# Optimization experiments

Hardware: AMD Instinct MI355X
Metric: run time of the kernel (lower is better)

## Reference

```python
import jax, jax.numpy as jnp
import numpy as np

DIM = 128
HEADS = 4
GN_GROUPS = 4
EPS = 1e-5


def setup_inputs() -> dict:
    key = jax.random.key(0)
    ks = jax.random.split(key, 6)
    B, C, H, W = 4, DIM, 64, 64
    x = jax.random.normal(ks[0], (B, C, H, W), dtype=jnp.float32)
    # 1x1 convs are channel matmuls: store as [out_ch, in_ch]
    w_qkv = jax.random.normal(ks[1], (3 * C, C), dtype=jnp.float32) * (C ** -0.5)
    w_out = jax.random.normal(ks[2], (C, C), dtype=jnp.float32) * (C ** -0.5)
    b_out = jax.random.normal(ks[3], (C,), dtype=jnp.float32) * 0.01
    gn_gamma = jnp.ones((C,), dtype=jnp.float32)
    gn_beta = jnp.zeros((C,), dtype=jnp.float32)
    return {"x": x, "w_qkv": w_qkv, "w_out": w_out, "b_out": b_out,
            "gn_gamma": gn_gamma, "gn_beta": gn_beta}


def _attention_block(x, w_qkv, w_out, b_out, gn_gamma, gn_beta):
    b, c, h, w = x.shape
    d = c // HEADS
    scale = d ** -0.5
    # 1x1 conv == per-pixel matmul over channels
    qkv = jnp.einsum('bchw,oc->bohw', x, w_qkv)  # [b, 3c, h, w]
    q, k, v = jnp.split(qkv, 3, axis=1)
    # 'b (h d) x y -> b h (x y) d'
    def to_heads(t):
        return t.reshape(b, HEADS, d, h * w).transpose(0, 1, 3, 2)  # [b, H, N, d]
    q, k, v = to_heads(q), to_heads(k), to_heads(v)
    dots = jnp.einsum('bhnd,bhmd->bhnm', q, k) * scale  # [b, H, N, N]
    attn = jax.nn.softmax(dots, axis=-1)
    out = jnp.einsum('bhnm,bhmd->bhnd', attn, v)  # [b, H, N, d]
    # 'b h (x y) d -> b (h d) x y'
    out = out.transpose(0, 1, 3, 2).reshape(b, c, h, w)
    # output 1x1 conv + bias
    out = jnp.einsum('bchw,oc->bohw', out, w_out) + b_out[None, :, None, None]
    # GroupNorm(4, c)
    g = out.reshape(b, GN_GROUPS, c // GN_GROUPS, h, w)
    mean = g.mean(axis=(2, 3, 4), keepdims=True)
    var = g.var(axis=(2, 3, 4), keepdims=True)
    g = (g - mean) * jax.lax.rsqrt(var + EPS)
    out = g.reshape(b, c, h, w) * gn_gamma[None, :, None, None] + gn_beta[None, :, None, None]
    return out + x


def reference(x, w_qkv, w_out, b_out, gn_gamma, gn_beta):
    return _attention_block(x, w_qkv, w_out, b_out, gn_gamma, gn_beta)
```

## Files before the change

### kernel.cpp

```cpp
#include <hip/hip_runtime.h>

#define DIM   128
#define NPIX  4096
#define DHEAD 32

using u16 = unsigned short;
typedef __attribute__((ext_vector_type(8))) short   short8;
typedef __attribute__((ext_vector_type(8))) u16     ushort8;
typedef __attribute__((ext_vector_type(4))) float   floatx4;
typedef __attribute__((ext_vector_type(2))) unsigned int uint2v;

#define SCL 0.25513899f

__device__ __forceinline__ float bf2f(u16 u) {
  union { unsigned int i; float f; } v; v.i = ((unsigned int)u) << 16; return v.f;
}
__device__ __forceinline__ u16 f2bf(float f) {
  union { unsigned int i; float f; } v; v.f = f;
  unsigned int i = v.i;
  return (u16)((i + 0x7FFFu + ((i >> 16) & 1u)) >> 16);
}
__device__ __forceinline__ unsigned int pk2bf(float a, float b) {
  union { float f; unsigned int u; } ua, ub; ua.f = a; ub.f = b;
  return __builtin_amdgcn_perm(ub.u, ua.u, 0x07060302u);
}

template<bool F32> __device__ __forceinline__ float ld1(const void* p, size_t i) {
  if constexpr (F32) return ((const float*)p)[i];
  else               return bf2f(((const u16*)p)[i]);
}
template<bool F32> __device__ __forceinline__ float4 ld4(const void* p, size_t i) {
  if constexpr (F32) {
    return *(const float4*)((const float*)p + i);
  } else {
    const ushort4 u = *(const ushort4*)((const u16*)p + i);
    return make_float4(bf2f(u.x), bf2f(u.y), bf2f(u.z), bf2f(u.w));
  }
}
template<bool F32> __device__ __forceinline__ void st4(void* p, size_t i, float4 v) {
  if constexpr (F32) {
    *(float4*)((float*)p + i) = v;
  } else {
    ushort4 u; u.x = f2bf(v.x); u.y = f2bf(v.y); u.z = f2bf(v.z); u.w = f2bf(v.w);
    *(ushort4*)((u16*)p + i) = u;
  }
}

__global__ void k_detect(const u16* __restrict__ x, int* __restrict__ flag,
                         float* __restrict__ S) {
  if (threadIdx.x < 40) S[threadIdx.x] = 0.f;
  if (threadIdx.x == 0 && blockIdx.x == 0) {
    int big = 0;
    for (int i = 0; i < 128; ++i) {
      const float v = bf2f(x[i]);
      if (!(fabsf(v) < 1e4f)) big = 1;
    }
    *flag = big;
  }
}

template<bool F32>
__global__ __launch_bounds__(256) void k_qkv(const void* __restrict__ x,
                                             const void* __restrict__ wqkv,
                                             u16* __restrict__ Q,
                                             u16* __restrict__ K,
                                             u16* __restrict__ V,
                                             const int* __restrict__ flag) {
  if (*flag != (F32 ? 1 : 0)) return;
  const int b = blockIdx.z, y = blockIdx.y, pt = blockIdx.x;
  const int tl = threadIdx.x;
  __shared__ float Ws[32 * 129];
  if (y < 8) {
    const int m = y >> 2, h = y & 3;
    const int ddq = tl & 3, pw = tl >> 2;
    const int rb = m * DIM + h * 32;
    for (int i = tl; i < 32 * DIM; i += 256)
      Ws[(i >> 7) * 129 + (i & 127)] =
          ld1<F32>(wqkv, (size_t)(rb + (i >> 7)) * DIM + (i & 127));
    __syncthreads();
    const int p0 = pt * 256 + pw * 4;
    float acc[8][4];
#pragma unroll
    for (int j = 0; j < 8; ++j) { acc[j][0] = acc[j][1] = acc[j][2] = acc[j][3] = 0.f; }
    const size_t xb = (size_t)b * DIM * NPIX + p0;
    for (int c = 0; c < DIM; ++c) {
      const float4 xv = ld4<F32>(x, xb + (size_t)c * NPIX);
#pragma unroll
      for (int j = 0; j < 8; ++j) {
        const float wv = Ws[(ddq * 8 + j) * 129 + c];
        acc[j][0] += wv * xv.x; acc[j][1] += wv * xv.y;
        acc[j][2] += wv * xv.z; acc[j][3] += wv * xv.w;
      }
    }
    u16* dst = (m == 0) ? Q : K;
    const float scl = (m == 0) ? 1.f : SCL;
    const int bh = b * 4 + h;
#pragma unroll
    for (int t = 0; t < 4; ++t) {
      ushort8 w8;
#pragma unroll
      for (int j = 0; j < 8; ++j) w8[j] = f2bf(acc[j][t] * scl);
      *(ushort8*)(dst + ((size_t)bh * NPIX + p0 + t) * DHEAD + ddq * 8) = w8;
    }
  } else {
    const int og = (y - 8) * 4 + (pt >> 2);
    const int ptv = pt & 3;
    for (int i = tl; i < 8 * DIM; i += 256)
      Ws[(i >> 7) * 129 + (i & 127)] =
          ld1<F32>(wqkv, (size_t)(2 * DIM + og * 8 + (i >> 7)) * DIM + (i & 127));
    __syncthreads();
    const int p0 = ptv * 1024 + tl * 4;
    float acc[8][4];
#pragma unroll
    for (int j = 0; j < 8; ++j) { acc[j][0] = acc[j][1] = acc[j][2] = acc[j][3] = 0.f; }
    const size_t xb = (size_t)b * DIM * NPIX + p0;
    for (int c = 0; c < DIM; ++c) {
      const float4 xv = ld4<F32>(x, xb + (size_t)c * NPIX);
#pragma unroll
      for (int j = 0; j < 8; ++j) {
        const float wv = Ws[j * 129 + c];
        acc[j][0] += wv * xv.x; acc[j][1] += wv * xv.y;
        acc[j][2] += wv * xv.z; acc[j][3] += wv * xv.w;
      }
    }
#pragma unroll
    for (int j = 0; j < 8; ++j) {
      const int c = og * 8 + j;
      ushort4 w4;
      w4.x = f2bf(acc[j][0]); w4.y = f2bf(acc[j][1]);
      w4.z = f2bf(acc[j][2]); w4.w = f2bf(acc[j][3]);
      *(ushort4*)(V + ((size_t)b * DIM + c) * NPIX + p0) = w4;
    }
  }
}

__device__ __forceinline__ short8 xform_p(unsigned c0, unsigned c1,
                                          unsigned c2, unsigned c3) {
  uint2v sw = __builtin_amdgcn_permlane32_swap(c0, c2, false, false);
  uint2v sx = __builtin_amdgcn_permlane16_swap(sw[0], sw[1], false, false);
  uint2v sy = __builtin_amdgcn_permlane32_swap(c1, c3, false, false);
  uint2v sz = __builtin_amdgcn_permlane16_swap(sy[0], sy[1], false, false);
  union { unsigned u[4]; short8 s; } r;
  r.u[0] = sx[0]; r.u[1] = sz[0]; r.u[2] = sx[1]; r.u[3] = sz[1];
  return r.s;
}

__global__ __launch_bounds__(512) void k_attn(const u16* __restrict__ Q,
                                              const u16* __restrict__ K,
                                              const u16* __restrict__ V,
                                              u16* __restrict__ O) {
  const int bh = blockIdx.y, qb = blockIdx.x;
  const int tid = threadIdx.x;
  const int wv = tid >> 6, lane = tid & 63;
  const int quad = lane >> 4, l15 = lane & 15;
  const int b = bh >> 2, h = bh & 3;

  __shared__ __align__(16) u16 Klds[2][64 * 40];
  __shared__ __align__(16) u16 Vlds[2][32 * 72];
  __shared__ __align__(16) u16 Olds[32 * 136];

  const int qtok0 = qb * 128 + wv * 16 + l15;
  const short8 qf = *(const short8*)(Q + ((size_t)bh * NPIX + qtok0) * DHEAD + quad * 8);

  floatx4 o00 = {0.f, 0.f, 0.f, 0.f}, o01 = {0.f, 0.f, 0.f, 0.f};
  float lp0 = 0.f;

  const int st = tid & 255;
  const bool isK = tid < 256;
  const int skey = st >> 2, sqt = st & 3;
  const int sdd = st >> 3, soc = st & 7;
  const u16* Gg = isK ? (K + ((size_t)bh * NPIX + skey) * DHEAD + sqt * 8)
                      : (V + ((size_t)(b * DIM + h * DHEAD + sdd)) * NPIX + soc * 8);
  u16* Ld0 = isK ? (Klds[0] + skey * 40 + sqt * 8) : (Vlds[0] + sdd * 72 + soc * 8);
  u16* Ld1 = isK ? (Klds[1] + skey * 40 + sqt * 8) : (Vlds[1] + sdd * 72 + soc * 8);
  const size_t gstride = isK ? (size_t)(64 * DHEAD) : (size_t)64;

  *(ushort8*)Ld0 = *(const ushort8*)Gg;

  for (int ch = 0; ch < 64; ++ch) {
    const int cur = ch & 1;
    __syncthreads();
    ushort8 pre;
    if (ch + 1 < 64) {
      pre = *(const ushort8*)(Gg + (size_t)(ch + 1) * gstride);
    }
#pragma unroll
    for (int kc = 0; kc < 2; ++kc) {
      unsigned ca[4];
#pragma unroll
      for (int s = 0; s < 2; ++s) {
        const int sub = kc * 2 + s;
        const short8 af = *(const short8*)(Klds[cur] + (sub * 16 + l15) * 40 + quad * 8);
        const floatx4 s0 = __builtin_amdgcn_mfma_f32_16x16x32_bf16(
            af, qf, (floatx4){0.f, 0.f, 0.f, 0.f}, 0, 0, 0);
        const float a0 = __builtin_amdgcn_exp2f(s0[0]);
        const float a1 = __builtin_amdgcn_exp2f(s0[1]);
        const float a2 = __builtin_amdgcn_exp2f(s0[2]);
        const float a3 = __builtin_amdgcn_exp2f(s0[3]);
        lp0 += (a0 + a1) + (a2 + a3);
        ca[s * 2 + 0] = pk2bf(a0, a1); ca[s * 2 + 1] = pk2bf(a2, a3);
      }
      const short8 pa = xform_p(ca[0], ca[1], ca[2], ca[3]);
      const short8 vb0 = *(const short8*)(Vlds[cur] + l15 * 72 + kc * 32 + quad * 8);
      const short8 vb1 = *(const short8*)(Vlds[cur] + (16 + l15) * 72 + kc * 32 + quad * 8);
      o00 = __builtin_amdgcn_mfma_f32_16x16x32_bf16(pa, vb0, o00, 0, 0, 0);
      o01 = __builtin_amdgcn_mfma_f32_16x16x32_bf16(pa, vb1, o01, 0, 0, 0);
    }
    if (ch + 1 < 64) {
      *(ushort8*)(cur ? Ld0 : Ld1) = pre;
    }
  }
  float l0 = lp0;
  l0 += __shfl_xor(l0, 16); l0 += __shfl_xor(l0, 32);
  float li[4];
#pragma unroll
  for (int r = 0; r < 4; ++r) {
    li[r] = 1.f / __shfl(l0, (lane & 48) | (quad * 4 + r));
  }
  uint2v w00, w01;
  w00[0] = (unsigned)f2bf(o00[0] * li[0]) | ((unsigned)f2bf(o00[1] * li[1]) << 16);
  w00[1] = (unsigned)f2bf(o00[2] * li[2]) | ((unsigned)f2bf(o00[3] * li[3]) << 16);
  w01[0] = (unsigned)f2bf(o01[0] * li[0]) | ((unsigned)f2bf(o01[1] * li[1]) << 16);
  w01[1] = (unsigned)f2bf(o01[2] * li[2]) | ((unsigned)f2bf(o01[3] * li[3]) << 16);
  __syncthreads();
  *(uint2v*)(Olds + l15 * 136 + wv * 16 + quad * 4) = w00;
  *(uint2v*)(Olds + (16 + l15) * 136 + wv * 16 + quad * 4) = w01;
  __syncthreads();
  const int d = tid >> 4, oc = tid & 15;
  u16* og = O + ((size_t)(b * DIM + h * DHEAD + d)) * NPIX + qb * 128;
  *(ushort8*)(og + oc * 8) = *(const ushort8*)(Olds + d * 136 + oc * 8);
}

template<bool F32>
__global__ __launch_bounds__(256) void k_proj(const u16* __restrict__ O,
                                              const void* __restrict__ wout,
                                              const void* __restrict__ bout,
                                              float* __restrict__ Y,
                                              float* __restrict__ Sred,
                                              const int* __restrict__ flag) {
  if (*flag != (F32 ? 1 : 0)) return;
  const int b = blockIdx.z, og = blockIdx.y, pt = blockIdx.x;
  const int tl = threadIdx.x;
  __shared__ float Ws[8][DIM];
  for (int i = tl; i < 8 * DIM; i += 256)
    Ws[i >> 7][i & 127] = ld1<F32>(wout, (size_t)(og * 8 + (i >> 7)) * DIM + (i & 127));
  __syncthreads();
  const int p0 = pt * 1024 + tl * 4;
  float acc[8][4];
#pragma unroll
  for (int j = 0; j < 8; ++j) { acc[j][0] = acc[j][1] = acc[j][2] = acc[j][3] = 0.f; }
  const u16* Ob = O + (size_t)b * DIM * NPIX + p0;
  for (int c = 0; c < DIM; ++c) {
    const ushort4 xv4 = *(const ushort4*)(Ob + (size_t)c * NPIX);
    const float x0 = bf2f(xv4.x), x1 = bf2f(xv4.y), x2 = bf2f(xv4.z), x3 = bf2f(xv4.w);
#pragma unroll
    for (int j = 0; j < 8; ++j) {
      const float wv = Ws[j][c];
      acc[j][0] += wv * x0; acc[j][1] += wv * x1;
      acc[j][2] += wv * x2; acc[j][3] += wv * x3;
    }
  }
  float s1 = 0.f, s2 = 0.f;
#pragma unroll
  for (int j = 0; j < 8; ++j) {
    const int o = og * 8 + j;
    const float bo = ld1<F32>(bout, o);
    float4 y4;
    y4.x = acc[j][0] + bo; y4.y = acc[j][1] + bo;
    y4.z = acc[j][2] + bo; y4.w = acc[j][3] + bo;
    *(float4*)(Y + ((size_t)b * DIM + o) * NPIX + p0) = y4;
    s1 += y4.x + y4.y + y4.z + y4.w;
    s2 += y4.x * y4.x + y4.y * y4.y + y4.z * y4.z + y4.w * y4.w;
  }
  __shared__ float red[2][256];
  red[0][tl] = s1; red[1][tl] = s2;
  __syncthreads();
  for (int off = 128; off >= 1; off >>= 1) {
    if (tl < off) { red[0][tl] += red[0][tl + off]; red[1][tl] += red[1][tl + off]; }
    __syncthreads();
  }
  if (tl == 0) {
    const int g = og >> 2;
    atomicAdd(&Sred[(b * 4 + g) * 2 + 0], red[0][0]);
    atomicAdd(&Sred[(b * 4 + g) * 2 + 1], red[1][0]);
  }
}

template<bool F32>
__global__ __launch_bounds__(256) void k_gn(const float* __restrict__ Y,
                                            const float* __restrict__ Sred,
                                            const void* __restrict__ x,
                                            const void* __restrict__ gamma,
                                            const void* __restrict__ beta,
                                            void* __restrict__ out,
                                            const int* __restrict__ flag) {
  if (*flag != (F32 ? 1 : 0)) return;
  const int idx = (blockIdx.x * 256 + threadIdx.x) * 4;
  const int b = idx >> 19;
  const int c = (idx >> 12) & 127;
  const int g = c >> 5;
  const float inv_n = 1.f / (32.f * 4096.f);
  const float s1 = Sred[(b * 4 + g) * 2 + 0];
  const float s2 = Sred[(b * 4 + g) * 2 + 1];
  const float mean = s1 * inv_n;
  const float var = s2 * inv_n - mean * mean;
  const float rs = rsqrtf(var + 1e-5f);
  const float ga = ld1<F32>(gamma, c) * rs;
  const float be = ld1<F32>(beta, c) - mean * ga;
  const float4 y4 = *(const float4*)(Y + idx);
  const float4 xv = ld4<F32>(x, idx);
  float4 r;
  r.x = y4.x * ga + be + xv.x;
  r.y = y4.y * ga + be + xv.y;
  r.z = y4.z * ga + be + xv.z;
  r.w = y4.w * ga + be + xv.w;
  st4<F32>(out, idx, r);
}

extern "C" void kernel_launch(void* const* d_in, const int* in_sizes, int n_in,
                              void* d_out, int out_size, void* d_ws, size_t ws_size,
                              hipStream_t stream) {
  const void* x     = d_in[0];
  const void* wqkv  = d_in[1];
  const void* wout  = d_in[2];
  const void* bout  = d_in[3];
  const void* gamma = d_in[4];
  const void* beta  = d_in[5];
  char* ws = (char*)d_ws;
  u16*   Q = (u16*)(ws + ((size_t)0  << 20));
  u16*   K = (u16*)(ws + ((size_t)8  << 20));
  u16*   V = (u16*)(ws + ((size_t)16 << 20));
  u16*   O = (u16*)(ws + ((size_t)24 << 20));
  float* Y = (float*)(ws + ((size_t)32 << 20));
  float* S = (float*)(ws + ((size_t)40 << 20));
  int*   F = (int*)(ws + ((size_t)40 << 20) + 128);

  k_detect<<<1, 64, 0, stream>>>((const u16*)x, F, S);

  k_qkv<false><<<dim3(16, 12, 4), 256, 0, stream>>>(x, wqkv, Q, K, V, F);
  k_qkv<true> <<<dim3(16, 12, 4), 256, 0, stream>>>(x, wqkv, Q, K, V, F);
  k_attn<<<dim3(32, 16), 512, 0, stream>>>(Q, K, V, O);
  k_proj<false><<<dim3(4, 16, 4), 256, 0, stream>>>(O, wout, bout, Y, S, F);
  k_proj<true> <<<dim3(4, 16, 4), 256, 0, stream>>>(O, wout, bout, Y, S, F);
  k_gn<false><<<2048, 256, 0, stream>>>(Y, S, x, gamma, beta, d_out, F);
  k_gn<true> <<<2048, 256, 0, stream>>>(Y, S, x, gamma, beta, d_out, F);
}
```

Before: 190.5 us.

## Halve attention and projection tile sizes and swizzle attention block order

The attention kernel now uses 256-thread blocks covering 64 query tokens instead of 512 threads covering 128, which doubles the grid to 1024 blocks. Each thread now stages both its K and V chunk. Block IDs are remapped so that neighbouring launched blocks fall on different batch-heads, spreading K/V reads across L2/XCDs. The projection kernel halves pixels per thread to double its grid. The aim is better CU occupancy and load balance across the 256 CUs, at the cost of each K/V tile being reloaded by twice as many blocks.

```diff
diff --git a/kernel.cpp b/kernel.cpp
--- a/kernel.cpp
+++ b/kernel.cpp
@@ -145,11 +145,13 @@
   return r.s;
 }
 
-__global__ __launch_bounds__(512) void k_attn(const u16* __restrict__ Q,
+__global__ __launch_bounds__(256) void k_attn(const u16* __restrict__ Q,
                                               const u16* __restrict__ K,
                                               const u16* __restrict__ V,
                                               u16* __restrict__ O) {
-  const int bh = blockIdx.y, qb = blockIdx.x;
+  const int id = blockIdx.y * 64 + blockIdx.x;
+  const int nid = (id & 7) * 128 + (id >> 3);
+  const int bh = nid >> 6, qb = nid & 63;
   const int tid = threadIdx.x;
   const int wv = tid >> 6, lane = tid & 63;
   const int quad = lane >> 4, l15 = lane & 15;
@@ -157,32 +159,33 @@
 
   __shared__ __align__(16) u16 Klds[2][64 * 40];
   __shared__ __align__(16) u16 Vlds[2][32 * 72];
-  __shared__ __align__(16) u16 Olds[32 * 136];
-
-  const int qtok0 = qb * 128 + wv * 16 + l15;
+  __shared__ __align__(16) u16 Olds[32 * 72];
+
+  const int qtok0 = qb * 64 + wv * 16 + l15;
   const short8 qf = *(const short8*)(Q + ((size_t)bh * NPIX + qtok0) * DHEAD + quad * 8);
 
   floatx4 o00 = {0.f, 0.f, 0.f, 0.f}, o01 = {0.f, 0.f, 0.f, 0.f};
   float lp0 = 0.f;
 
-  const int st = tid & 255;
-  const bool isK = tid < 256;
-  const int skey = st >> 2, sqt = st & 3;
-  const int sdd = st >> 3, soc = st & 7;
-  const u16* Gg = isK ? (K + ((size_t)bh * NPIX + skey) * DHEAD + sqt * 8)
-                      : (V + ((size_t)(b * DIM + h * DHEAD + sdd)) * NPIX + soc * 8);
-  u16* Ld0 = isK ? (Klds[0] + skey * 40 + sqt * 8) : (Vlds[0] + sdd * 72 + soc * 8);
-  u16* Ld1 = isK ? (Klds[1] + skey * 40 + sqt * 8) : (Vlds[1] + sdd * 72 + soc * 8);
-  const size_t gstride = isK ? (size_t)(64 * DHEAD) : (size_t)64;
-
-  *(ushort8*)Ld0 = *(const ushort8*)Gg;
+  const int skey = tid >> 2, sqt = tid & 3;
+  const int sdd = tid >> 3, soc = tid & 7;
+  const u16* Kg = K + ((size_t)bh * NPIX + skey) * DHEAD + sqt * 8;
+  const u16* Vg = V + ((size_t)(b * DIM + h * DHEAD + sdd)) * NPIX + soc * 8;
+
+  {
+    const ushort8 k0 = *(const ushort8*)Kg;
+    const ushort8 v0 = *(const ushort8*)Vg;
+    *(ushort8*)(Klds[0] + skey * 40 + sqt * 8) = k0;
+    *(ushort8*)(Vlds[0] + sdd * 72 + soc * 8) = v0;
+  }
 
   for (int ch = 0; ch < 64; ++ch) {
-    const int cur = ch & 1;
+    const int cur = ch & 1, nxt = cur ^ 1;
     __syncthreads();
-    ushort8 pre;
+    ushort8 kpre, vpre;
     if (ch + 1 < 64) {
-      pre = *(const ushort8*)(Gg + (size_t)(ch + 1) * gstride);
+      kpre = *(const ushort8*)(Kg + (size_t)(ch + 1) * 64 * DHEAD);
+      vpre = *(const ushort8*)(Vg + (ch + 1) * 64);
     }
 #pragma unroll
     for (int kc = 0; kc < 2; ++kc) {
@@ -207,7 +210,8 @@
       o01 = __builtin_amdgcn_mfma_f32_16x16x32_bf16(pa, vb1, o01, 0, 0, 0);
     }
     if (ch + 1 < 64) {
-      *(ushort8*)(cur ? Ld0 : Ld1) = pre;
+      *(ushort8*)(Klds[nxt] + skey * 40 + sqt * 8) = kpre;
+      *(ushort8*)(Vlds[nxt] + sdd * 72 + soc * 8) = vpre;
     }
   }
   float l0 = lp0;
@@ -223,12 +227,12 @@
   w01[0] = (unsigned)f2bf(o01[0] * li[0]) | ((unsigned)f2bf(o01[1] * li[1]) << 16);
   w01[1] = (unsigned)f2bf(o01[2] * li[2]) | ((unsigned)f2bf(o01[3] * li[3]) << 16);
   __syncthreads();
-  *(uint2v*)(Olds + l15 * 136 + wv * 16 + quad * 4) = w00;
-  *(uint2v*)(Olds + (16 + l15) * 136 + wv * 16 + quad * 4) = w01;
+  *(uint2v*)(Olds + l15 * 72 + wv * 16 + quad * 4) = w00;
+  *(uint2v*)(Olds + (16 + l15) * 72 + wv * 16 + quad * 4) = w01;
   __syncthreads();
-  const int d = tid >> 4, oc = tid & 15;
-  u16* og = O + ((size_t)(b * DIM + h * DHEAD + d)) * NPIX + qb * 128;
-  *(ushort8*)(og + oc * 8) = *(const ushort8*)(Olds + d * 136 + oc * 8);
+  const int d = tid >> 3, oc = tid & 7;
+  u16* og = O + ((size_t)(b * DIM + h * DHEAD + d)) * NPIX + qb * 64;
+  *(ushort8*)(og + oc * 8) = *(const ushort8*)(Olds + d * 72 + oc * 8);
 }
 
 template<bool F32>
@@ -245,19 +249,18 @@
   for (int i = tl; i < 8 * DIM; i += 256)
     Ws[i >> 7][i & 127] = ld1<F32>(wout, (size_t)(og * 8 + (i >> 7)) * DIM + (i & 127));
   __syncthreads();
-  const int p0 = pt * 1024 + tl * 4;
-  float acc[8][4];
-#pragma unroll
-  for (int j = 0; j < 8; ++j) { acc[j][0] = acc[j][1] = acc[j][2] = acc[j][3] = 0.f; }
+  const int p0 = pt * 512 + tl * 2;
+  float acc[8][2];
+#pragma unroll
+  for (int j = 0; j < 8; ++j) { acc[j][0] = acc[j][1] = 0.f; }
   const u16* Ob = O + (size_t)b * DIM * NPIX + p0;
   for (int c = 0; c < DIM; ++c) {
-    const ushort4 xv4 = *(const ushort4*)(Ob + (size_t)c * NPIX);
-    const float x0 = bf2f(xv4.x), x1 = bf2f(xv4.y), x2 = bf2f(xv4.z), x3 = bf2f(xv4.w);
+    const ushort2 xv2 = *(const ushort2*)(Ob + (size_t)c * NPIX);
+    const float x0 = bf2f(xv2.x), x1 = bf2f(xv2.y);
 #pragma unroll
     for (int j = 0; j < 8; ++j) {
       const float wv = Ws[j][c];
       acc[j][0] += wv * x0; acc[j][1] += wv * x1;
-      acc[j][2] += wv * x2; acc[j][3] += wv * x3;
     }
   }
   float s1 = 0.f, s2 = 0.f;
@@ -265,12 +268,11 @@
   for (int j = 0; j < 8; ++j) {
     const int o = og * 8 + j;
     const float bo = ld1<F32>(bout, o);
-    float4 y4;
-    y4.x = acc[j][0] + bo; y4.y = acc[j][1] + bo;
-    y4.z = acc[j][2] + bo; y4.w = acc[j][3] + bo;
-    *(float4*)(Y + ((size_t)b * DIM + o) * NPIX + p0) = y4;
-    s1 += y4.x + y4.y + y4.z + y4.w;
-    s2 += y4.x * y4.x + y4.y * y4.y + y4.z * y4.z + y4.w * y4.w;
+    float2 y2;
+    y2.x = acc[j][0] + bo; y2.y = acc[j][1] + bo;
+    *(float2*)(Y + ((size_t)b * DIM + o) * NPIX + p0) = y2;
+    s1 += y2.x + y2.y;
+    s2 += y2.x * y2.x + y2.y * y2.y;
   }
   __shared__ float red[2][256];
   red[0][tl] = s1; red[1][tl] = s2;
@@ -339,9 +341,9 @@
 
   k_qkv<false><<<dim3(16, 12, 4), 256, 0, stream>>>(x, wqkv, Q, K, V, F);
   k_qkv<true> <<<dim3(16, 12, 4), 256, 0, stream>>>(x, wqkv, Q, K, V, F);
-  k_attn<<<dim3(32, 16), 512, 0, stream>>>(Q, K, V, O);
-  k_proj<false><<<dim3(4, 16, 4), 256, 0, stream>>>(O, wout, bout, Y, S, F);
-  k_proj<true> <<<dim3(4, 16, 4), 256, 0, stream>>>(O, wout, bout, Y, S, F);
+  k_attn<<<dim3(64, 16), 256, 0, stream>>>(Q, K, V, O);
+  k_proj<false><<<dim3(8, 16, 4), 256, 0, stream>>>(O, wout, bout, Y, S, F);
+  k_proj<true> <<<dim3(8, 16, 4), 256, 0, stream>>>(O, wout, bout, Y, S, F);
   k_gn<false><<<2048, 256, 0, stream>>>(Y, S, x, gamma, beta, d_out, F);
   k_gn<true> <<<2048, 256, 0, stream>>>(Y, S, x, gamma, beta, d_out, F);
 }
```

Result: slower. 200.3 us (+5.1%).

## Enlarge attention key chunks, compute row sums via MFMA, remap blocks, split projection finer

Applied to the files above, without the earlier changes.

The attention kernel now stages 128 keys per iteration instead of 64, which halves the number of barrier-separated loop trips. Softmax denominators now come from an extra MFMA against a ones vector rather than scalar adds followed by cross-lane shuffles. Block IDs are remapped so that blocks sharing the same batch and head are spread across XCDs, and the projection kernel uses twice as many blocks with two pixels per thread to raise occupancy. The trade-offs are more LDS per block, an extra MFMA per step, and row sums computed from bf16-rounded probabilities.

```diff
diff --git a/kernel.cpp b/kernel.cpp
--- a/kernel.cpp
+++ b/kernel.cpp
@@ -149,21 +149,25 @@
                                               const u16* __restrict__ K,
                                               const u16* __restrict__ V,
                                               u16* __restrict__ O) {
-  const int bh = blockIdx.y, qb = blockIdx.x;
+  const int id = blockIdx.y * 32 + blockIdx.x;
+  const int nid = (id & 7) * 64 + (id >> 3);
+  const int bh = nid >> 5, qb = nid & 31;
   const int tid = threadIdx.x;
   const int wv = tid >> 6, lane = tid & 63;
   const int quad = lane >> 4, l15 = lane & 15;
   const int b = bh >> 2, h = bh & 3;
 
-  __shared__ __align__(16) u16 Klds[2][64 * 40];
-  __shared__ __align__(16) u16 Vlds[2][32 * 72];
+  __shared__ __align__(16) u16 Klds[2][128 * 40];
+  __shared__ __align__(16) u16 Vlds[2][32 * 136];
   __shared__ __align__(16) u16 Olds[32 * 136];
 
   const int qtok0 = qb * 128 + wv * 16 + l15;
   const short8 qf = *(const short8*)(Q + ((size_t)bh * NPIX + qtok0) * DHEAD + quad * 8);
 
   floatx4 o00 = {0.f, 0.f, 0.f, 0.f}, o01 = {0.f, 0.f, 0.f, 0.f};
-  float lp0 = 0.f;
+  floatx4 ol  = {0.f, 0.f, 0.f, 0.f};
+  const short8 onesf = {(short)0x3F80, (short)0x3F80, (short)0x3F80, (short)0x3F80,
+                        (short)0x3F80, (short)0x3F80, (short)0x3F80, (short)0x3F80};
 
   const int st = tid & 255;
   const bool isK = tid < 256;
@@ -171,21 +175,26 @@
   const int sdd = st >> 3, soc = st & 7;
   const u16* Gg = isK ? (K + ((size_t)bh * NPIX + skey) * DHEAD + sqt * 8)
                       : (V + ((size_t)(b * DIM + h * DHEAD + sdd)) * NPIX + soc * 8);
-  u16* Ld0 = isK ? (Klds[0] + skey * 40 + sqt * 8) : (Vlds[0] + sdd * 72 + soc * 8);
-  u16* Ld1 = isK ? (Klds[1] + skey * 40 + sqt * 8) : (Vlds[1] + sdd * 72 + soc * 8);
-  const size_t gstride = isK ? (size_t)(64 * DHEAD) : (size_t)64;
-
-  *(ushort8*)Ld0 = *(const ushort8*)Gg;
-
-  for (int ch = 0; ch < 64; ++ch) {
+  u16* Ld0 = isK ? (Klds[0] + skey * 40 + sqt * 8) : (Vlds[0] + sdd * 136 + soc * 8);
+  u16* Ld1 = isK ? (Klds[1] + skey * 40 + sqt * 8) : (Vlds[1] + sdd * 136 + soc * 8);
+  const size_t gstep = isK ? (size_t)(128 * DHEAD) : (size_t)128;
+  const size_t goff2 = isK ? (size_t)(64 * DHEAD)  : (size_t)64;
+  const int    loff2 = isK ? (64 * 40) : 64;
+
+  *(ushort8*)Ld0           = *(const ushort8*)Gg;
+  *(ushort8*)(Ld0 + loff2) = *(const ushort8*)(Gg + goff2);
+
+  for (int ch = 0; ch < 32; ++ch) {
     const int cur = ch & 1;
     __syncthreads();
-    ushort8 pre;
-    if (ch + 1 < 64) {
-      pre = *(const ushort8*)(Gg + (size_t)(ch + 1) * gstride);
-    }
-#pragma unroll
-    for (int kc = 0; kc < 2; ++kc) {
+    ushort8 pre0, pre1;
+    if (ch + 1 < 32) {
+      const u16* gb = Gg + (size_t)(ch + 1) * gstep;
+      pre0 = *(const ushort8*)gb;
+      pre1 = *(const ushort8*)(gb + goff2);
+    }
+#pragma unroll
+    for (int kc = 0; kc < 4; ++kc) {
       unsigned ca[4];
 #pragma unroll
       for (int s = 0; s < 2; ++s) {
@@ -197,26 +206,24 @@
         const float a1 = __builtin_amdgcn_exp2f(s0[1]);
         const float a2 = __builtin_amdgcn_exp2f(s0[2]);
         const float a3 = __builtin_amdgcn_exp2f(s0[3]);
-        lp0 += (a0 + a1) + (a2 + a3);
         ca[s * 2 + 0] = pk2bf(a0, a1); ca[s * 2 + 1] = pk2bf(a2, a3);
       }
       const short8 pa = xform_p(ca[0], ca[1], ca[2], ca[3]);
-      const short8 vb0 = *(const short8*)(Vlds[cur] + l15 * 72 + kc * 32 + quad * 8);
-      const short8 vb1 = *(const short8*)(Vlds[cur] + (16 + l15) * 72 + kc * 32 + quad * 8);
+      const short8 vb0 = *(const short8*)(Vlds[cur] + l15 * 136 + kc * 32 + quad * 8);
+      const short8 vb1 = *(const short8*)(Vlds[cur] + (16 + l15) * 136 + kc * 32 + quad * 8);
       o00 = __builtin_amdgcn_mfma_f32_16x16x32_bf16(pa, vb0, o00, 0, 0, 0);
       o01 = __builtin_amdgcn_mfma_f32_16x16x32_bf16(pa, vb1, o01, 0, 0, 0);
-    }
-    if (ch + 1 < 64) {
-      *(ushort8*)(cur ? Ld0 : Ld1) = pre;
-    }
-  }
-  float l0 = lp0;
-  l0 += __shfl_xor(l0, 16); l0 += __shfl_xor(l0, 32);
+      ol  = __builtin_amdgcn_mfma_f32_16x16x32_bf16(pa, onesf, ol, 0, 0, 0);
+    }
+    if (ch + 1 < 32) {
+      u16* dst = cur ? Ld0 : Ld1;
+      *(ushort8*)dst           = pre0;
+      *(ushort8*)(dst + loff2) = pre1;
+    }
+  }
   float li[4];
 #pragma unroll
-  for (int r = 0; r < 4; ++r) {
-    li[r] = 1.f / __shfl(l0, (lane & 48) | (quad * 4 + r));
-  }
+  for (int r = 0; r < 4; ++r) li[r] = 1.f / ol[r];
   uint2v w00, w01;
   w00[0] = (unsigned)f2bf(o00[0] * li[0]) | ((unsigned)f2bf(o00[1] * li[1]) << 16);
   w00[1] = (unsigned)f2bf(o00[2] * li[2]) | ((unsigned)f2bf(o00[3] * li[3]) << 16);
@@ -245,19 +252,18 @@
   for (int i = tl; i < 8 * DIM; i += 256)
     Ws[i >> 7][i & 127] = ld1<F32>(wout, (size_t)(og * 8 + (i >> 7)) * DIM + (i & 127));
   __syncthreads();
-  const int p0 = pt * 1024 + tl * 4;
-  float acc[8][4];
-#pragma unroll
-  for (int j = 0; j < 8; ++j) { acc[j][0] = acc[j][1] = acc[j][2] = acc[j][3] = 0.f; }
+  const int p0 = pt * 512 + tl * 2;
+  float acc[8][2];
+#pragma unroll
+  for (int j = 0; j < 8; ++j) { acc[j][0] = acc[j][1] = 0.f; }
   const u16* Ob = O + (size_t)b * DIM * NPIX + p0;
   for (int c = 0; c < DIM; ++c) {
-    const ushort4 xv4 = *(const ushort4*)(Ob + (size_t)c * NPIX);
-    const float x0 = bf2f(xv4.x), x1 = bf2f(xv4.y), x2 = bf2f(xv4.z), x3 = bf2f(xv4.w);
+    const ushort2 xv2 = *(const ushort2*)(Ob + (size_t)c * NPIX);
+    const float x0 = bf2f(xv2.x), x1 = bf2f(xv2.y);
 #pragma unroll
     for (int j = 0; j < 8; ++j) {
       const float wv = Ws[j][c];
       acc[j][0] += wv * x0; acc[j][1] += wv * x1;
-      acc[j][2] += wv * x2; acc[j][3] += wv * x3;
     }
   }
   float s1 = 0.f, s2 = 0.f;
@@ -265,12 +271,11 @@
   for (int j = 0; j < 8; ++j) {
     const int o = og * 8 + j;
     const float bo = ld1<F32>(bout, o);
-    float4 y4;
-    y4.x = acc[j][0] + bo; y4.y = acc[j][1] + bo;
-    y4.z = acc[j][2] + bo; y4.w = acc[j][3] + bo;
-    *(float4*)(Y + ((size_t)b * DIM + o) * NPIX + p0) = y4;
-    s1 += y4.x + y4.y + y4.z + y4.w;
-    s2 += y4.x * y4.x + y4.y * y4.y + y4.z * y4.z + y4.w * y4.w;
+    float2 y2;
+    y2.x = acc[j][0] + bo; y2.y = acc[j][1] + bo;
+    *(float2*)(Y + ((size_t)b * DIM + o) * NPIX + p0) = y2;
+    s1 += y2.x + y2.y;
+    s2 += y2.x * y2.x + y2.y * y2.y;
   }
   __shared__ float red[2][256];
   red[0][tl] = s1; red[1][tl] = s2;
@@ -340,8 +345,8 @@
   k_qkv<false><<<dim3(16, 12, 4), 256, 0, stream>>>(x, wqkv, Q, K, V, F);
   k_qkv<true> <<<dim3(16, 12, 4), 256, 0, stream>>>(x, wqkv, Q, K, V, F);
   k_attn<<<dim3(32, 16), 512, 0, stream>>>(Q, K, V, O);
-  k_proj<false><<<dim3(4, 16, 4), 256, 0, stream>>>(O, wout, bout, Y, S, F);
-  k_proj<true> <<<dim3(4, 16, 4), 256, 0, stream>>>(O, wout, bout, Y, S, F);
+  k_proj<false><<<dim3(8, 16, 4), 256, 0, stream>>>(O, wout, bout, Y, S, F);
+  k_proj<true> <<<dim3(8, 16, 4), 256, 0, stream>>>(O, wout, bout, Y, S, F);
   k_gn<false><<<2048, 256, 0, stream>>>(Y, S, x, gamma, beta, d_out, F);
   k_gn<true> <<<2048, 256, 0, stream>>>(Y, S, x, gamma, beta, d_out, F);
 }
```

New measurement: 182.1 us. 1.05x faster.
